# Performance work log

Measured on AMD Instinct MI355X. Metric: run time of the kernel, lower is better.

The kernel has to match this reference:

```python
import jax, jax.numpy as jnp
import numpy as np


def setup_inputs() -> dict:
    key = jax.random.key(0)
    ks = jax.random.split(key, 6)
    B, F, C = 2048, 512, 64
    t_feat = jax.random.normal(ks[0], (B, F), dtype=jnp.float32)
    f_feat = jax.random.normal(ks[1], (B, F), dtype=jnp.float32)
    # proj Linear(F*F -> C); scale like torch default init (~1/sqrt(fan_in))
    W_proj = jax.random.normal(ks[2], (C, F * F), dtype=jnp.float32) / np.sqrt(F * F)
    b_proj = jnp.zeros((C,), dtype=jnp.float32)
    W1 = jax.random.normal(ks[3], (32, C), dtype=jnp.float32) / np.sqrt(C)
    b1 = jnp.zeros((32,), dtype=jnp.float32)
    W2 = jax.random.normal(ks[4], (1, 32), dtype=jnp.float32) / np.sqrt(32)
    b2 = jnp.zeros((1,), dtype=jnp.float32)
    return {"t_feat": t_feat, "f_feat": f_feat, "W_proj": W_proj, "b_proj": b_proj,
            "W1": W1, "b1": b1, "W2": W2, "b2": b2}


def reference(t_feat, f_feat, W_proj, b_proj, W1, b1, W2, b2):
    B, F = t_feat.shape
    C = W_proj.shape[0]
    # corr[b,i,j] = t[b,i] * f[b,j]; proj = corr_flat @ W_proj.T + b_proj.
    # Equivalent bilinear form computed WITHOUT materializing the (B,F,F) outer product:
    Wr = W_proj.reshape(C, F, F)            # W_proj[c, i*F + j] -> Wr[c,i,j]
    tmp = jnp.einsum('bi,cij->bcj', t_feat, Wr)   # (B, C, F)
    proj = jnp.einsum('bcj,bj->bc', tmp, f_feat) + b_proj  # (B, C)
    h = jax.nn.relu(proj)
    # GRL is identity in forward
    h2 = jax.nn.relu(h @ W1.T + b1)          # (B, 32)
    logit = h2 @ W2.T + b2                   # (B, 1)
    return logit
```

## Files before the change

### kernel.cpp

```cpp
#include <hip/hip_runtime.h>
#include <hip/hip_bf16.h>
#include <stdint.h>

#define BATCH 2048
#define FDIM 512
#define CDIM 64

typedef unsigned short ushort_t;
typedef __attribute__((ext_vector_type(8))) short short8;
typedef __attribute__((ext_vector_type(4))) float f32x4;

__device__ __forceinline__ ushort_t f2bf(float x) {
    union { float f; uint32_t u; } v; v.f = x;
    uint32_t u = v.u;
    uint32_t r = u + 0x7FFFu + ((u >> 16) & 1u);
    return (ushort_t)(r >> 16);
}
__device__ __forceinline__ float bf2f(ushort_t u) {
    union { float f; uint32_t v; } x; x.v = ((uint32_t)u) << 16; return x.f;
}

__global__ void convert_kernel(const float* __restrict__ src, ushort_t* __restrict__ dst) {
    int idx = blockIdx.x * 256 + threadIdx.x;
    float4 v0 = ((const float4*)src)[idx * 2];
    float4 v1 = ((const float4*)src)[idx * 2 + 1];
    ushort_t p[8] = { f2bf(v0.x), f2bf(v0.y), f2bf(v0.z), f2bf(v0.w),
                      f2bf(v1.x), f2bf(v1.y), f2bf(v1.z), f2bf(v1.w) };
    *(uint4*)&dst[idx * 8] = *(uint4*)p;
}

__global__ void convert_ft_kernel(const float* __restrict__ f, ushort_t* __restrict__ f16,
                                  const float* __restrict__ t, ushort_t* __restrict__ t16) {
    int blk = blockIdx.x;
    const float* src = (blk < 512) ? f : t;
    ushort_t* dst    = (blk < 512) ? f16 : t16;
    int idx = (blk & 511) * 256 + threadIdx.x;
    float4 v0 = ((const float4*)src)[idx * 2];
    float4 v1 = ((const float4*)src)[idx * 2 + 1];
    ushort_t p[8] = { f2bf(v0.x), f2bf(v0.y), f2bf(v0.z), f2bf(v0.w),
                      f2bf(v1.x), f2bf(v1.y), f2bf(v1.z), f2bf(v1.w) };
    *(uint4*)&dst[idx * 8] = *(uint4*)p;
}

#define AS3(p) ((__attribute__((address_space(3))) void*)(p))
#define AS1(p) ((const __attribute__((address_space(1))) void*)(p))

__launch_bounds__(256, 2)
__global__ void gemm_fused_kernel(const ushort_t* __restrict__ f16,
                                  const ushort_t* __restrict__ Wb,
                                  const ushort_t* __restrict__ t16,
                                  float* __restrict__ part) {
    __shared__ ushort_t As[128 * 32];
    __shared__ ushort_t Bs[128 * 32];
    __shared__ float scratch[256];

    const int tid  = threadIdx.x;
    const int wave = tid >> 6;
    const int lane = tid & 63;
    const int l15  = lane & 15;
    const int lg   = lane >> 4;

    const int b0 = blockIdx.x * 128;
    const int n0 = blockIdx.y * 128;

    const int m_base = (wave >> 1) * 64;
    const int nh     = wave & 1;
    const int n_base = nh * 64;

    f32x4 acc[4][4];
    #pragma unroll
    for (int mi = 0; mi < 4; mi++)
        #pragma unroll
        for (int ni = 0; ni < 4; ni++)
            acc[mi][ni] = (f32x4){0.f, 0.f, 0.f, 0.f};

    const int p    = tid >> 2;
    const int cph  = tid & 3;
    const int cg   = cph ^ ((p >> 1) & 3);
    const int nrot = ((p & 15) << 2) | (p >> 4);

    const ushort_t* gA0 = f16 + (size_t)(b0 + p) * FDIM + cg * 8;
    const ushort_t* gA1 = f16 + (size_t)(b0 + 64 + p) * FDIM + cg * 8;
    const ushort_t* gB0 = Wb + (size_t)(n0 + nrot) * FDIM + cg * 8;
    const ushort_t* gB1 = Wb + (size_t)(n0 + 64 + nrot) * FDIM + cg * 8;

    for (int k0 = 0; k0 < FDIM; k0 += 32) {
        __builtin_amdgcn_global_load_lds(AS1(gA0 + k0), AS3(&As[0 * 2048 + wave * 512]), 16, 0, 0);
        __builtin_amdgcn_global_load_lds(AS1(gA1 + k0), AS3(&As[1 * 2048 + wave * 512]), 16, 0, 0);
        __builtin_amdgcn_global_load_lds(AS1(gB0 + k0), AS3(&Bs[0 * 2048 + wave * 512]), 16, 0, 0);
        __builtin_amdgcn_global_load_lds(AS1(gB1 + k0), AS3(&Bs[1 * 2048 + wave * 512]), 16, 0, 0);
        __syncthreads();

        short8 a[4], b[4];
        #pragma unroll
        for (int mi = 0; mi < 4; mi++) {
            int r = m_base + mi * 16 + l15;
            a[mi] = *(const short8*)&As[r * 32 + (lg ^ ((r >> 1) & 3)) * 8];
        }
        #pragma unroll
        for (int ni = 0; ni < 4; ni++) {
            int q = n_base + ni * 16 + l15;
            b[ni] = *(const short8*)&Bs[q * 32 + (lg ^ ((q >> 1) & 3)) * 8];
        }

        #pragma unroll
        for (int mi = 0; mi < 4; mi++)
            #pragma unroll
            for (int ni = 0; ni < 4; ni++)
                acc[mi][ni] = __builtin_amdgcn_mfma_f32_16x16x32_bf16(a[mi], b[ni], acc[mi][ni], 0, 0, 0);

        __syncthreads();
    }

    const int c  = n0 >> 9;
    const int iq = (n0 >> 7) & 3;
    const int i_base = (n0 & 511) + n_base + l15 * 4;

    #pragma unroll
    for (int mi = 0; mi < 4; mi++) {
        #pragma unroll
        for (int r = 0; r < 4; r++) {
            int b_idx = b0 + m_base + mi * 16 + lg * 4 + r;
            ushort4 tv = *(const ushort4*)&t16[(size_t)b_idx * FDIM + i_base];
            float sv = acc[mi][0][r] * bf2f(tv.x) + acc[mi][1][r] * bf2f(tv.y)
                     + acc[mi][2][r] * bf2f(tv.z) + acc[mi][3][r] * bf2f(tv.w);
            sv += __shfl_xor(sv, 1, 64);
            sv += __shfl_xor(sv, 2, 64);
            sv += __shfl_xor(sv, 4, 64);
            sv += __shfl_xor(sv, 8, 64);
            if (l15 == 0)
                scratch[(m_base + mi * 16 + lg * 4 + r) * 2 + nh] = sv;
        }
    }
    __syncthreads();
    if (tid < 128) {
        float v = scratch[tid * 2] + scratch[tid * 2 + 1];
        part[(((size_t)(b0 + tid)) * 64 + c) * 4 + iq] = v;
    }
}

__global__ void mlp_kernel(const float* __restrict__ part,
                           const float* __restrict__ b_proj,
                           const float* __restrict__ W1, const float* __restrict__ b1,
                           const float* __restrict__ W2, const float* __restrict__ b2,
                           float* __restrict__ out) {
    __shared__ float h[8][64];
    const int tid = threadIdx.x;
    const int bl  = tid >> 5;
    const int o   = tid & 31;
    const int b   = blockIdx.x * 8 + bl;

    #pragma unroll
    for (int c = o; c < 64; c += 32) {
        float4 v = *(const float4*)&part[(((size_t)b * 64 + c)) * 4];
        float sv = v.x + v.y + v.z + v.w + b_proj[c];
        h[bl][c] = sv > 0.f ? sv : 0.f;
    }
    __syncthreads();

    float sv = b1[o];
    #pragma unroll
    for (int c = 0; c < 64; c++) sv += h[bl][c] * W1[o * 64 + c];
    float v = (sv > 0.f ? sv : 0.f) * W2[o];
    v += __shfl_xor(v, 1, 32);
    v += __shfl_xor(v, 2, 32);
    v += __shfl_xor(v, 4, 32);
    v += __shfl_xor(v, 8, 32);
    v += __shfl_xor(v, 16, 32);
    if (o == 0) out[b] = v + b2[0];
}

extern "C" void kernel_launch(void* const* d_in, const int* in_sizes, int n_in,
                              void* d_out, int out_size, void* d_ws, size_t ws_size,
                              hipStream_t stream) {
    const float* t_feat = (const float*)d_in[0];
    const float* f_feat = (const float*)d_in[1];
    const float* W_proj = (const float*)d_in[2];
    const float* b_proj = (const float*)d_in[3];
    const float* W1     = (const float*)d_in[4];
    const float* b1     = (const float*)d_in[5];
    const float* W2     = (const float*)d_in[6];
    const float* b2     = (const float*)d_in[7];
    float* out = (float*)d_out;

    uint8_t* ws = (uint8_t*)d_ws;
    ushort_t* Wb   = (ushort_t*)(ws);
    ushort_t* f16  = (ushort_t*)(ws + 33554432);
    ushort_t* t16  = (ushort_t*)(ws + 33554432 + 2097152);
    float*    part = (float*)(ws + 33554432 + 2 * 2097152);

    convert_kernel<<<dim3((CDIM * FDIM * FDIM) / 2048), dim3(256), 0, stream>>>(W_proj, Wb);
    convert_ft_kernel<<<dim3(1024), dim3(256), 0, stream>>>(f_feat, f16, t_feat, t16);

    gemm_fused_kernel<<<dim3(BATCH / 128, (CDIM * FDIM) / 128), dim3(256), 0, stream>>>(
        f16, Wb, t16, part);

    mlp_kernel<<<dim3(BATCH / 8), dim3(256), 0, stream>>>(part, b_proj, W1, b1, W2, b2, out);
}
```

Baseline: 211.1 us.

## Double-buffer 256x256 GEMM tiles with phased prefetch and merge conversion kernels

The GEMM moves from 128x128 tiles with a single LDS buffer to 256x256 tiles run by 8 waves. It double-buffers BK=64 k-tiles and issues the global-to-LDS prefetch of the next tile inside phases interleaved with the MFMA work, using explicit barriers, waitcnt and setprio. A block-index swizzle improves L2 reuse, the three conversion kernels are merged into one launch, and the partial-sum layout shrinks from four to two slices per channel. The aim is to hide load latency behind compute and raise arithmetic intensity, at the cost of more registers and LDS (64KB+) and fragile hand scheduling.

```diff
diff --git a/kernel.cpp b/kernel.cpp
--- a/kernel.cpp
+++ b/kernel.cpp
@@ -5,6 +5,8 @@
 #define BATCH 2048
 #define FDIM 512
 #define CDIM 64
+#define BK 64
+#define NKT (FDIM / BK)
 
 typedef unsigned short ushort_t;
 typedef __attribute__((ext_vector_type(8))) short short8;
@@ -20,8 +22,14 @@
     union { float f; uint32_t v; } x; x.v = ((uint32_t)u) << 16; return x.f;
 }
 
-__global__ void convert_kernel(const float* __restrict__ src, ushort_t* __restrict__ dst) {
-    int idx = blockIdx.x * 256 + threadIdx.x;
+__global__ void convert_all_kernel(const float* __restrict__ W, ushort_t* __restrict__ Wb,
+                                   const float* __restrict__ f, ushort_t* __restrict__ f16,
+                                   const float* __restrict__ t, ushort_t* __restrict__ t16) {
+    int blk = blockIdx.x;
+    const float* src; ushort_t* dst; int idx;
+    if (blk < 8192)      { src = W; dst = Wb;  idx = blk * 256 + threadIdx.x; }
+    else if (blk < 8704) { src = f; dst = f16; idx = (blk - 8192) * 256 + threadIdx.x; }
+    else                 { src = t; dst = t16; idx = (blk - 8704) * 256 + threadIdx.x; }
     float4 v0 = ((const float4*)src)[idx * 2];
     float4 v1 = ((const float4*)src)[idx * 2 + 1];
     ushort_t p[8] = { f2bf(v0.x), f2bf(v0.y), f2bf(v0.z), f2bf(v0.w),
@@ -29,113 +37,149 @@
     *(uint4*)&dst[idx * 8] = *(uint4*)p;
 }
 
-__global__ void convert_ft_kernel(const float* __restrict__ f, ushort_t* __restrict__ f16,
-                                  const float* __restrict__ t, ushort_t* __restrict__ t16) {
-    int blk = blockIdx.x;
-    const float* src = (blk < 512) ? f : t;
-    ushort_t* dst    = (blk < 512) ? f16 : t16;
-    int idx = (blk & 511) * 256 + threadIdx.x;
-    float4 v0 = ((const float4*)src)[idx * 2];
-    float4 v1 = ((const float4*)src)[idx * 2 + 1];
-    ushort_t p[8] = { f2bf(v0.x), f2bf(v0.y), f2bf(v0.z), f2bf(v0.w),
-                      f2bf(v1.x), f2bf(v1.y), f2bf(v1.z), f2bf(v1.w) };
-    *(uint4*)&dst[idx * 8] = *(uint4*)p;
-}
-
 #define AS3(p) ((__attribute__((address_space(3))) void*)(p))
 #define AS1(p) ((const __attribute__((address_space(1))) void*)(p))
 
-__launch_bounds__(256, 2)
+
+#define STAGE_A(buf, ksub, kelem)                                                   \
+    { _Pragma("unroll")                                                             \
+      for (int l = 0; l < 2; l++)                                                   \
+        __builtin_amdgcn_global_load_lds(AS1(gA[l] + (kelem) + (ksub) * 32),        \
+            AS3(&AsB[buf][ksub][l * 4096 + wave * 512]), 16, 0, 0); }
+
+#define STAGE_B(buf, ksub, kelem)                                                   \
+    { _Pragma("unroll")                                                             \
+      for (int l = 0; l < 2; l++)                                                   \
+        __builtin_amdgcn_global_load_lds(AS1(gB[l] + (kelem) + (ksub) * 32),        \
+            AS3(&BsB[buf][ksub][l * 4096 + wave * 512]), 16, 0, 0); }
+
+#define LOADB4(buf, ksub)                                                           \
+    { _Pragma("unroll")                                                             \
+      for (int ni = 0; ni < 4; ni++)                                                \
+        bv[ni] = *(const short8*)&BsB[buf][ksub][b_off[ni]]; }
+
+#define VMW4 asm volatile("s_waitcnt vmcnt(4)" ::: "memory");
+
+#define PHASE(buf, ksub, mibase, EXTRA, STG, VMW)                                   \
+    { _Pragma("unroll")                                                             \
+      for (int mi = 0; mi < 4; mi++)                                                \
+        av[mi] = *(const short8*)&AsB[buf][ksub][a_off[(mibase) + mi]];             \
+      EXTRA                                                                         \
+      STG                                                                           \
+      __builtin_amdgcn_s_barrier();                                                 \
+      asm volatile("s_waitcnt lgkmcnt(0)" ::: "memory");                            \
+      __builtin_amdgcn_sched_barrier(0);                                            \
+      __builtin_amdgcn_s_setprio(1);                                                \
+      _Pragma("unroll")                                                             \
+      for (int mi = 0; mi < 4; mi++) {                                              \
+        _Pragma("unroll")                                                           \
+        for (int ni = 0; ni < 4; ni++)                                              \
+          acc[(mibase) + mi][ni] = __builtin_amdgcn_mfma_f32_16x16x32_bf16(         \
+              av[mi], bv[ni], acc[(mibase) + mi][ni], 0, 0, 0);                     \
+      }                                                                             \
+      __builtin_amdgcn_s_setprio(0);                                                \
+      VMW                                                                           \
+      __builtin_amdgcn_s_barrier();                                                 \
+      asm volatile("" ::: "memory"); }
+
+#define DO_KTILE(buf, nk)                                                           \
+    PHASE(buf, 0, 0, LOADB4(buf, 0), STAGE_A((buf) ^ 1, 0, nk), )                   \
+    PHASE(buf, 0, 4, , STAGE_B((buf) ^ 1, 0, nk), VMW4)                             \
+    PHASE(buf, 1, 0, LOADB4(buf, 1), STAGE_A((buf) ^ 1, 1, nk), )                   \
+    PHASE(buf, 1, 4, , STAGE_B((buf) ^ 1, 1, nk), VMW4)
+
+__launch_bounds__(512, 2)
 __global__ void gemm_fused_kernel(const ushort_t* __restrict__ f16,
                                   const ushort_t* __restrict__ Wb,
                                   const ushort_t* __restrict__ t16,
                                   float* __restrict__ part) {
-    __shared__ ushort_t As[128 * 32];
-    __shared__ ushort_t Bs[128 * 32];
-    __shared__ float scratch[256];
+    __shared__ ushort_t AsB[2][2][256 * 32];
+    __shared__ ushort_t BsB[2][2][256 * 32];
+    __shared__ float scratch[256 * 4];
 
     const int tid  = threadIdx.x;
     const int wave = tid >> 6;
     const int lane = tid & 63;
     const int l15  = lane & 15;
     const int lg   = lane >> 4;
-
-    const int b0 = blockIdx.x * 128;
-    const int n0 = blockIdx.y * 128;
-
-    const int m_base = (wave >> 1) * 64;
-    const int nh     = wave & 1;
-    const int n_base = nh * 64;
-
-    f32x4 acc[4][4];
-    #pragma unroll
-    for (int mi = 0; mi < 4; mi++)
+    const int wm   = wave >> 2;
+    const int wn   = wave & 3;
+
+    const int swz = (blockIdx.x & 7) * 128 + (blockIdx.x >> 3);
+    const int by  = swz >> 3;
+    const int bx  = swz & 7;
+    const int b0  = bx * 256;
+    const int n0  = by * 256;
+
+    const ushort_t* gA[2];
+    const ushort_t* gB[2];
+    #pragma unroll
+    for (int l = 0; l < 2; l++) {
+        int s   = l * 512 + tid;
+        int row = s >> 2;
+        int cg  = (s & 3) ^ ((row >> 1) & 3);
+        gA[l] = f16 + (size_t)(b0 + row) * FDIM + cg * 8;
+        int bq = (row & ~63) | ((row & 15) << 2) | ((row >> 4) & 3);
+        gB[l] = Wb + (size_t)(n0 + bq) * FDIM + cg * 8;
+    }
+
+    int a_off[8], b_off[4];
+    const int cx = (lg ^ ((l15 >> 1) & 3)) * 8;
+    #pragma unroll
+    for (int mi = 0; mi < 8; mi++) {
+        int r = wm * 128 + mi * 16 + l15;
+        a_off[mi] = r * 32 + cx;
+    }
+    #pragma unroll
+    for (int ni = 0; ni < 4; ni++) {
+        int q = wn * 64 + ni * 16 + l15;
+        b_off[ni] = q * 32 + cx;
+    }
+
+    f32x4 acc[8][4];
+    #pragma unroll
+    for (int mi = 0; mi < 8; mi++)
         #pragma unroll
         for (int ni = 0; ni < 4; ni++)
             acc[mi][ni] = (f32x4){0.f, 0.f, 0.f, 0.f};
 
-    const int p    = tid >> 2;
-    const int cph  = tid & 3;
-    const int cg   = cph ^ ((p >> 1) & 3);
-    const int nrot = ((p & 15) << 2) | (p >> 4);
-
-    const ushort_t* gA0 = f16 + (size_t)(b0 + p) * FDIM + cg * 8;
-    const ushort_t* gA1 = f16 + (size_t)(b0 + 64 + p) * FDIM + cg * 8;
-    const ushort_t* gB0 = Wb + (size_t)(n0 + nrot) * FDIM + cg * 8;
-    const ushort_t* gB1 = Wb + (size_t)(n0 + 64 + nrot) * FDIM + cg * 8;
-
-    for (int k0 = 0; k0 < FDIM; k0 += 32) {
-        __builtin_amdgcn_global_load_lds(AS1(gA0 + k0), AS3(&As[0 * 2048 + wave * 512]), 16, 0, 0);
-        __builtin_amdgcn_global_load_lds(AS1(gA1 + k0), AS3(&As[1 * 2048 + wave * 512]), 16, 0, 0);
-        __builtin_amdgcn_global_load_lds(AS1(gB0 + k0), AS3(&Bs[0 * 2048 + wave * 512]), 16, 0, 0);
-        __builtin_amdgcn_global_load_lds(AS1(gB1 + k0), AS3(&Bs[1 * 2048 + wave * 512]), 16, 0, 0);
-        __syncthreads();
-
-        short8 a[4], b[4];
-        #pragma unroll
-        for (int mi = 0; mi < 4; mi++) {
-            int r = m_base + mi * 16 + l15;
-            a[mi] = *(const short8*)&As[r * 32 + (lg ^ ((r >> 1) & 3)) * 8];
-        }
-        #pragma unroll
-        for (int ni = 0; ni < 4; ni++) {
-            int q = n_base + ni * 16 + l15;
-            b[ni] = *(const short8*)&Bs[q * 32 + (lg ^ ((q >> 1) & 3)) * 8];
-        }
-
-        #pragma unroll
-        for (int mi = 0; mi < 4; mi++)
-            #pragma unroll
-            for (int ni = 0; ni < 4; ni++)
-                acc[mi][ni] = __builtin_amdgcn_mfma_f32_16x16x32_bf16(a[mi], b[ni], acc[mi][ni], 0, 0, 0);
-
-        __syncthreads();
-    }
-
-    const int c  = n0 >> 9;
-    const int iq = (n0 >> 7) & 3;
-    const int i_base = (n0 & 511) + n_base + l15 * 4;
-
-    #pragma unroll
-    for (int mi = 0; mi < 4; mi++) {
+    short8 av[4], bv[4];
+
+    STAGE_A(0, 0, 0)
+    STAGE_B(0, 0, 0)
+    STAGE_A(0, 1, 0)
+    STAGE_B(0, 1, 0)
+    __syncthreads();
+
+    for (int kt2 = 0; kt2 < 4; kt2++) {
+        const int nk1 = (kt2 * 2 + 1) * BK;
+        const int nk2 = (kt2 < 3) ? (kt2 * 2 + 2) * BK : 0;
+        DO_KTILE(0, nk1)
+        DO_KTILE(1, nk2)
+    }
+
+    const int c     = n0 >> 9;
+    const int half  = (n0 >> 8) & 1;
+    const int ibase = (n0 & 511) + wn * 64 + l15 * 4;
+    #pragma unroll
+    for (int mi = 0; mi < 8; mi++) {
+        const int row_blk = wm * 128 + mi * 16 + lg * 4;
         #pragma unroll
         for (int r = 0; r < 4; r++) {
-            int b_idx = b0 + m_base + mi * 16 + lg * 4 + r;
-            ushort4 tv = *(const ushort4*)&t16[(size_t)b_idx * FDIM + i_base];
+            ushort4 tv = *(const ushort4*)&t16[(size_t)(b0 + row_blk + r) * FDIM + ibase];
             float sv = acc[mi][0][r] * bf2f(tv.x) + acc[mi][1][r] * bf2f(tv.y)
                      + acc[mi][2][r] * bf2f(tv.z) + acc[mi][3][r] * bf2f(tv.w);
             sv += __shfl_xor(sv, 1, 64);
             sv += __shfl_xor(sv, 2, 64);
             sv += __shfl_xor(sv, 4, 64);
             sv += __shfl_xor(sv, 8, 64);
-            if (l15 == 0)
-                scratch[(m_base + mi * 16 + lg * 4 + r) * 2 + nh] = sv;
+            if (l15 == 0) scratch[(row_blk + r) * 4 + wn] = sv;
         }
     }
     __syncthreads();
-    if (tid < 128) {
-        float v = scratch[tid * 2] + scratch[tid * 2 + 1];
-        part[(((size_t)(b0 + tid)) * 64 + c) * 4 + iq] = v;
+    if (tid < 256) {
+        float4 s4 = *(const float4*)&scratch[tid * 4];
+        part[((size_t)(b0 + tid) * CDIM + c) * 2 + half] = s4.x + s4.y + s4.z + s4.w;
     }
 }
 
@@ -152,8 +196,8 @@
 
     #pragma unroll
     for (int c = o; c < 64; c += 32) {
-        float4 v = *(const float4*)&part[(((size_t)b * 64 + c)) * 4];
-        float sv = v.x + v.y + v.z + v.w + b_proj[c];
+        float2 v = *(const float2*)&part[((size_t)b * 64 + c) * 2];
+        float sv = v.x + v.y + b_proj[c];
         h[bl][c] = sv > 0.f ? sv : 0.f;
     }
     __syncthreads();
@@ -189,11 +233,9 @@
     ushort_t* t16  = (ushort_t*)(ws + 33554432 + 2097152);
     float*    part = (float*)(ws + 33554432 + 2 * 2097152);
 
-    convert_kernel<<<dim3((CDIM * FDIM * FDIM) / 2048), dim3(256), 0, stream>>>(W_proj, Wb);
-    convert_ft_kernel<<<dim3(1024), dim3(256), 0, stream>>>(f_feat, f16, t_feat, t16);
-
-    gemm_fused_kernel<<<dim3(BATCH / 128, (CDIM * FDIM) / 128), dim3(256), 0, stream>>>(
-        f16, Wb, t16, part);
+    convert_all_kernel<<<dim3(9216), dim3(256), 0, stream>>>(W_proj, Wb, f_feat, f16, t_feat, t16);
+
+    gemm_fused_kernel<<<dim3(1024), dim3(512), 0, stream>>>(f16, Wb, t16, part);
 
     mlp_kernel<<<dim3(BATCH / 8), dim3(256), 0, stream>>>(part, b_proj, W1, b1, W2, b2, out);
 }
```

After: 237.3 us. 1.12x slower.

## Load GEMM operands straight to registers with double buffering, XCD-aware block mapping, merged conversions

Applied to the files above, without the earlier changes.

Drops the LDS staging in the bilinear GEMM. Each wave now loads its A and B fragments directly from global memory into registers, double-buffered across K steps, with no barriers inside the K loop. Blocks are remapped onto a 1D grid so that each XCD takes a contiguous range of W column tiles for L2 reuse, and occupancy is raised to 3 blocks per CU. The two fp32-to-bf16 conversion kernels are merged into one launch. In exchange, the per-wave global loads are redundant and less coalesced (the 16-byte B row loads are strided), and register pressure rises.

```diff
diff --git a/kernel.cpp b/kernel.cpp
--- a/kernel.cpp
+++ b/kernel.cpp
@@ -20,8 +20,14 @@
     union { float f; uint32_t v; } x; x.v = ((uint32_t)u) << 16; return x.f;
 }
 
-__global__ void convert_kernel(const float* __restrict__ src, ushort_t* __restrict__ dst) {
-    int idx = blockIdx.x * 256 + threadIdx.x;
+__global__ void convert_all_kernel(const float* __restrict__ W, ushort_t* __restrict__ Wb,
+                                   const float* __restrict__ f, ushort_t* __restrict__ f16,
+                                   const float* __restrict__ t, ushort_t* __restrict__ t16) {
+    int blk = blockIdx.x;
+    const float* src; ushort_t* dst; int idx;
+    if (blk < 8192)      { src = W; dst = Wb;  idx = blk * 256 + threadIdx.x; }
+    else if (blk < 8704) { src = f; dst = f16; idx = (blk - 8192) * 256 + threadIdx.x; }
+    else                 { src = t; dst = t16; idx = (blk - 8704) * 256 + threadIdx.x; }
     float4 v0 = ((const float4*)src)[idx * 2];
     float4 v1 = ((const float4*)src)[idx * 2 + 1];
     ushort_t p[8] = { f2bf(v0.x), f2bf(v0.y), f2bf(v0.z), f2bf(v0.w),
@@ -29,43 +35,52 @@
     *(uint4*)&dst[idx * 8] = *(uint4*)p;
 }
 
-__global__ void convert_ft_kernel(const float* __restrict__ f, ushort_t* __restrict__ f16,
-                                  const float* __restrict__ t, ushort_t* __restrict__ t16) {
-    int blk = blockIdx.x;
-    const float* src = (blk < 512) ? f : t;
-    ushort_t* dst    = (blk < 512) ? f16 : t16;
-    int idx = (blk & 511) * 256 + threadIdx.x;
-    float4 v0 = ((const float4*)src)[idx * 2];
-    float4 v1 = ((const float4*)src)[idx * 2 + 1];
-    ushort_t p[8] = { f2bf(v0.x), f2bf(v0.y), f2bf(v0.z), f2bf(v0.w),
-                      f2bf(v1.x), f2bf(v1.y), f2bf(v1.z), f2bf(v1.w) };
-    *(uint4*)&dst[idx * 8] = *(uint4*)p;
-}
 
-#define AS3(p) ((__attribute__((address_space(3))) void*)(p))
-#define AS1(p) ((const __attribute__((address_space(1))) void*)(p))
+#define LOADK(Ad, Bd, koff)                                                         \
+    { _Pragma("unroll")                                                             \
+      for (int mi = 0; mi < 4; mi++) Ad[mi] = *(const short8*)(pA[mi] + (koff));    \
+      _Pragma("unroll")                                                             \
+      for (int ni = 0; ni < 4; ni++) Bd[ni] = *(const short8*)(pB[ni] + (koff)); }
 
-__launch_bounds__(256, 2)
+#define MFMAK(Av, Bv)                                                               \
+    { _Pragma("unroll")                                                             \
+      for (int mi = 0; mi < 4; mi++) {                                              \
+        _Pragma("unroll")                                                           \
+        for (int ni = 0; ni < 4; ni++)                                              \
+          acc[mi][ni] = __builtin_amdgcn_mfma_f32_16x16x32_bf16(                    \
+              Av[mi], Bv[ni], acc[mi][ni], 0, 0, 0);                                \
+      } }
+
+__launch_bounds__(256, 3)
 __global__ void gemm_fused_kernel(const ushort_t* __restrict__ f16,
                                   const ushort_t* __restrict__ Wb,
                                   const ushort_t* __restrict__ t16,
                                   float* __restrict__ part) {
-    __shared__ ushort_t As[128 * 32];
-    __shared__ ushort_t Bs[128 * 32];
-    __shared__ float scratch[256];
+    __shared__ float scratch[128 * 2];
 
     const int tid  = threadIdx.x;
     const int wave = tid >> 6;
     const int lane = tid & 63;
     const int l15  = lane & 15;
     const int lg   = lane >> 4;
+    const int wm   = wave >> 1;
+    const int wn   = wave & 1;
 
-    const int b0 = blockIdx.x * 128;
-    const int n0 = blockIdx.y * 128;
+    const int xcd = blockIdx.x & 7;
+    const int idx = blockIdx.x >> 3;
+    const int bx  = idx & 15;
+    const int by  = xcd * 32 + (idx >> 4);
+    const int b0  = bx * 128;
+    const int n0  = by * 128;
 
-    const int m_base = (wave >> 1) * 64;
-    const int nh     = wave & 1;
-    const int n_base = nh * 64;
+    const ushort_t* pA[4];
+    const ushort_t* pB[4];
+    #pragma unroll
+    for (int mi = 0; mi < 4; mi++)
+        pA[mi] = f16 + (size_t)(b0 + wm * 64 + mi * 16 + l15) * FDIM + lg * 8;
+    #pragma unroll
+    for (int ni = 0; ni < 4; ni++)
+        pB[ni] = Wb + (size_t)(n0 + wn * 64 + l15 * 4 + ni) * FDIM + lg * 8;
 
     f32x4 acc[4][4];
     #pragma unroll
@@ -74,68 +89,39 @@
         for (int ni = 0; ni < 4; ni++)
             acc[mi][ni] = (f32x4){0.f, 0.f, 0.f, 0.f};
 
-    const int p    = tid >> 2;
-    const int cph  = tid & 3;
-    const int cg   = cph ^ ((p >> 1) & 3);
-    const int nrot = ((p & 15) << 2) | (p >> 4);
+    short8 A0[4], B0[4], A1[4], B1[4];
 
-    const ushort_t* gA0 = f16 + (size_t)(b0 + p) * FDIM + cg * 8;
-    const ushort_t* gA1 = f16 + (size_t)(b0 + 64 + p) * FDIM + cg * 8;
-    const ushort_t* gB0 = Wb + (size_t)(n0 + nrot) * FDIM + cg * 8;
-    const ushort_t* gB1 = Wb + (size_t)(n0 + 64 + nrot) * FDIM + cg * 8;
-
-    for (int k0 = 0; k0 < FDIM; k0 += 32) {
-        __builtin_amdgcn_global_load_lds(AS1(gA0 + k0), AS3(&As[0 * 2048 + wave * 512]), 16, 0, 0);
-        __builtin_amdgcn_global_load_lds(AS1(gA1 + k0), AS3(&As[1 * 2048 + wave * 512]), 16, 0, 0);
-        __builtin_amdgcn_global_load_lds(AS1(gB0 + k0), AS3(&Bs[0 * 2048 + wave * 512]), 16, 0, 0);
-        __builtin_amdgcn_global_load_lds(AS1(gB1 + k0), AS3(&Bs[1 * 2048 + wave * 512]), 16, 0, 0);
-        __syncthreads();
-
-        short8 a[4], b[4];
-        #pragma unroll
-        for (int mi = 0; mi < 4; mi++) {
-            int r = m_base + mi * 16 + l15;
-            a[mi] = *(const short8*)&As[r * 32 + (lg ^ ((r >> 1) & 3)) * 8];
-        }
-        #pragma unroll
-        for (int ni = 0; ni < 4; ni++) {
-            int q = n_base + ni * 16 + l15;
-            b[ni] = *(const short8*)&Bs[q * 32 + (lg ^ ((q >> 1) & 3)) * 8];
-        }
-
-        #pragma unroll
-        for (int mi = 0; mi < 4; mi++)
-            #pragma unroll
-            for (int ni = 0; ni < 4; ni++)
-                acc[mi][ni] = __builtin_amdgcn_mfma_f32_16x16x32_bf16(a[mi], b[ni], acc[mi][ni], 0, 0, 0);
-
-        __syncthreads();
+    LOADK(A0, B0, 0)
+    #pragma unroll 1
+    for (int k = 0; k < FDIM; k += 64) {
+        LOADK(A1, B1, k + 32)
+        MFMAK(A0, B0)
+        LOADK(A0, B0, (k + 64) & 511)
+        MFMAK(A1, B1)
     }
 
-    const int c  = n0 >> 9;
-    const int iq = (n0 >> 7) & 3;
-    const int i_base = (n0 & 511) + n_base + l15 * 4;
-
+    const int c      = n0 >> 9;
+    const int iq     = (n0 >> 7) & 3;
+    const int i_base = (n0 & 511) + wn * 64 + l15 * 4;
     #pragma unroll
     for (int mi = 0; mi < 4; mi++) {
+        const int row_blk = wm * 64 + mi * 16 + lg * 4;
         #pragma unroll
         for (int r = 0; r < 4; r++) {
-            int b_idx = b0 + m_base + mi * 16 + lg * 4 + r;
-            ushort4 tv = *(const ushort4*)&t16[(size_t)b_idx * FDIM + i_base];
+            ushort4 tv = *(const ushort4*)&t16[(size_t)(b0 + row_blk + r) * FDIM + i_base];
             float sv = acc[mi][0][r] * bf2f(tv.x) + acc[mi][1][r] * bf2f(tv.y)
                      + acc[mi][2][r] * bf2f(tv.z) + acc[mi][3][r] * bf2f(tv.w);
             sv += __shfl_xor(sv, 1, 64);
             sv += __shfl_xor(sv, 2, 64);
             sv += __shfl_xor(sv, 4, 64);
             sv += __shfl_xor(sv, 8, 64);
-            if (l15 == 0)
-                scratch[(m_base + mi * 16 + lg * 4 + r) * 2 + nh] = sv;
+            if (l15 == 0) scratch[(row_blk + r) * 2 + wn] = sv;
         }
     }
     __syncthreads();
     if (tid < 128) {
-        float v = scratch[tid * 2] + scratch[tid * 2 + 1];
-        part[(((size_t)(b0 + tid)) * 64 + c) * 4 + iq] = v;
+        float2 s2 = *(const float2*)&scratch[tid * 2];
+        part[(((size_t)(b0 + tid)) * CDIM + c) * 4 + iq] = s2.x + s2.y;
     }
 }
 
@@ -189,10 +175,9 @@
     ushort_t* t16  = (ushort_t*)(ws + 33554432 + 2097152);
     float*    part = (float*)(ws + 33554432 + 2 * 2097152);
 
-    convert_kernel<<<dim3((CDIM * FDIM * FDIM) / 2048), dim3(256), 0, stream>>>(W_proj, Wb);
-    convert_ft_kernel<<<dim3(1024), dim3(256), 0, stream>>>(f_feat, f16, t_feat, t16);
+    convert_all_kernel<<<dim3(9216), dim3(256), 0, stream>>>(W_proj, Wb, f_feat, f16, t_feat, t16);
 
-    gemm_fused_kernel<<<dim3(BATCH / 128, (CDIM * FDIM) / 128), dim3(256), 0, stream>>>(
+    gemm_fused_kernel<<<dim3((BATCH / 128) * ((CDIM * FDIM) / 128)), dim3(256), 0, stream>>>(
         f16, Wb, t16, part);
 
     mlp_kernel<<<dim3(BATCH / 8), dim3(256), 0, stream>>>(part, b_proj, W1, b1, W2, b2, out);
```

New measurement: 355.9 us. 1.69x slower.

## Double-buffer GEMM LDS tiles, remap blocks per XCD, merge convert kernels

Applied to the files above, without the earlier changes.

The GEMM main loop now uses two LDS buffers, so the global-to-LDS loads for the next K tile are issued before the MFMAs on the current tile, and each step needs one barrier instead of two. The grid is flattened to 1D and remapped so each XCD gets a contiguous range of W_proj column tiles, which should improve L2 reuse of the weight tiles. Launch bounds rise to 4 blocks per CU, which limits register use. The three fp32-to-bf16 conversion launches are merged into one kernel to save launch overhead. The extra LDS and the tighter register budget could lower occupancy or cause spills.

```diff
diff --git a/kernel.cpp b/kernel.cpp
--- a/kernel.cpp
+++ b/kernel.cpp
@@ -20,8 +20,14 @@
     union { float f; uint32_t v; } x; x.v = ((uint32_t)u) << 16; return x.f;
 }
 
-__global__ void convert_kernel(const float* __restrict__ src, ushort_t* __restrict__ dst) {
-    int idx = blockIdx.x * 256 + threadIdx.x;
+__global__ void convert_all_kernel(const float* __restrict__ W, ushort_t* __restrict__ Wb,
+                                   const float* __restrict__ f, ushort_t* __restrict__ f16,
+                                   const float* __restrict__ t, ushort_t* __restrict__ t16) {
+    int blk = blockIdx.x;
+    const float* src; ushort_t* dst; int idx;
+    if (blk < 8192)      { src = W; dst = Wb;  idx = blk * 256 + threadIdx.x; }
+    else if (blk < 8704) { src = f; dst = f16; idx = (blk - 8192) * 256 + threadIdx.x; }
+    else                 { src = t; dst = t16; idx = (blk - 8704) * 256 + threadIdx.x; }
     float4 v0 = ((const float4*)src)[idx * 2];
     float4 v1 = ((const float4*)src)[idx * 2 + 1];
     ushort_t p[8] = { f2bf(v0.x), f2bf(v0.y), f2bf(v0.z), f2bf(v0.w),
@@ -29,29 +35,37 @@
     *(uint4*)&dst[idx * 8] = *(uint4*)p;
 }
 
-__global__ void convert_ft_kernel(const float* __restrict__ f, ushort_t* __restrict__ f16,
-                                  const float* __restrict__ t, ushort_t* __restrict__ t16) {
-    int blk = blockIdx.x;
-    const float* src = (blk < 512) ? f : t;
-    ushort_t* dst    = (blk < 512) ? f16 : t16;
-    int idx = (blk & 511) * 256 + threadIdx.x;
-    float4 v0 = ((const float4*)src)[idx * 2];
-    float4 v1 = ((const float4*)src)[idx * 2 + 1];
-    ushort_t p[8] = { f2bf(v0.x), f2bf(v0.y), f2bf(v0.z), f2bf(v0.w),
-                      f2bf(v1.x), f2bf(v1.y), f2bf(v1.z), f2bf(v1.w) };
-    *(uint4*)&dst[idx * 8] = *(uint4*)p;
-}
-
 #define AS3(p) ((__attribute__((address_space(3))) void*)(p))
 #define AS1(p) ((const __attribute__((address_space(1))) void*)(p))
 
-__launch_bounds__(256, 2)
+
+#define STAGE(bi, kt)                                                               \
+    __builtin_amdgcn_global_load_lds(AS1(gA0 + (kt) * 32), AS3(&As[bi][0 * 2048 + wave * 512]), 16, 0, 0); \
+    __builtin_amdgcn_global_load_lds(AS1(gA1 + (kt) * 32), AS3(&As[bi][1 * 2048 + wave * 512]), 16, 0, 0); \
+    __builtin_amdgcn_global_load_lds(AS1(gB0 + (kt) * 32), AS3(&Bs[bi][0 * 2048 + wave * 512]), 16, 0, 0); \
+    __builtin_amdgcn_global_load_lds(AS1(gB1 + (kt) * 32), AS3(&Bs[bi][1 * 2048 + wave * 512]), 16, 0, 0);
+
+#define COMPUTE(bi)                                                                 \
+    { short8 a[4], b[4];                                                            \
+      _Pragma("unroll")                                                             \
+      for (int mi = 0; mi < 4; mi++) a[mi] = *(const short8*)&As[bi][a_off[mi]];    \
+      _Pragma("unroll")                                                             \
+      for (int ni = 0; ni < 4; ni++) b[ni] = *(const short8*)&Bs[bi][b_off[ni]];    \
+      _Pragma("unroll")                                                             \
+      for (int mi = 0; mi < 4; mi++) {                                              \
+        _Pragma("unroll")                                                           \
+        for (int ni = 0; ni < 4; ni++)                                              \
+          acc[mi][ni] = __builtin_amdgcn_mfma_f32_16x16x32_bf16(                    \
+              a[mi], b[ni], acc[mi][ni], 0, 0, 0);                                  \
+      } }
+
+__launch_bounds__(256, 4)
 __global__ void gemm_fused_kernel(const ushort_t* __restrict__ f16,
                                   const ushort_t* __restrict__ Wb,
                                   const ushort_t* __restrict__ t16,
                                   float* __restrict__ part) {
-    __shared__ ushort_t As[128 * 32];
-    __shared__ ushort_t Bs[128 * 32];
+    __shared__ ushort_t As[2][128 * 32];
+    __shared__ ushort_t Bs[2][128 * 32];
     __shared__ float scratch[256];
 
     const int tid  = threadIdx.x;
@@ -60,12 +74,38 @@
     const int l15  = lane & 15;
     const int lg   = lane >> 4;
 
-    const int b0 = blockIdx.x * 128;
-    const int n0 = blockIdx.y * 128;
-
     const int m_base = (wave >> 1) * 64;
     const int nh     = wave & 1;
     const int n_base = nh * 64;
+
+    const int xcd = blockIdx.x & 7;
+    const int idx = blockIdx.x >> 3;
+    const int bx  = idx & 15;
+    const int by  = xcd * 32 + (idx >> 4);
+    const int b0  = bx * 128;
+    const int n0  = by * 128;
+
+    const int p    = tid >> 2;
+    const int cph  = tid & 3;
+    const int cg   = cph ^ ((p >> 1) & 3);
+    const int nrot = ((p & 15) << 2) | (p >> 4);
+
+    const ushort_t* gA0 = f16 + (size_t)(b0 + p) * FDIM + cg * 8;
+    const ushort_t* gA1 = f16 + (size_t)(b0 + 64 + p) * FDIM + cg * 8;
+    const ushort_t* gB0 = Wb + (size_t)(n0 + nrot) * FDIM + cg * 8;
+    const ushort_t* gB1 = Wb + (size_t)(n0 + 64 + nrot) * FDIM + cg * 8;
+
+    int a_off[4], b_off[4];
+    #pragma unroll
+    for (int mi = 0; mi < 4; mi++) {
+        int r = m_base + mi * 16 + l15;
+        a_off[mi] = r * 32 + (lg ^ ((r >> 1) & 3)) * 8;
+    }
+    #pragma unroll
+    for (int ni = 0; ni < 4; ni++) {
+        int q = n_base + ni * 16 + l15;
+        b_off[ni] = q * 32 + (lg ^ ((q >> 1) & 3)) * 8;
+    }
 
     f32x4 acc[4][4];
     #pragma unroll
@@ -74,43 +114,16 @@
         for (int ni = 0; ni < 4; ni++)
             acc[mi][ni] = (f32x4){0.f, 0.f, 0.f, 0.f};
 
-    const int p    = tid >> 2;
-    const int cph  = tid & 3;
-    const int cg   = cph ^ ((p >> 1) & 3);
-    const int nrot = ((p & 15) << 2) | (p >> 4);
-
-    const ushort_t* gA0 = f16 + (size_t)(b0 + p) * FDIM + cg * 8;
-    const ushort_t* gA1 = f16 + (size_t)(b0 + 64 + p) * FDIM + cg * 8;
-    const ushort_t* gB0 = Wb + (size_t)(n0 + nrot) * FDIM + cg * 8;
-    const ushort_t* gB1 = Wb + (size_t)(n0 + 64 + nrot) * FDIM + cg * 8;
-
-    for (int k0 = 0; k0 < FDIM; k0 += 32) {
-        __builtin_amdgcn_global_load_lds(AS1(gA0 + k0), AS3(&As[0 * 2048 + wave * 512]), 16, 0, 0);
-        __builtin_amdgcn_global_load_lds(AS1(gA1 + k0), AS3(&As[1 * 2048 + wave * 512]), 16, 0, 0);
-        __builtin_amdgcn_global_load_lds(AS1(gB0 + k0), AS3(&Bs[0 * 2048 + wave * 512]), 16, 0, 0);
-        __builtin_amdgcn_global_load_lds(AS1(gB1 + k0), AS3(&Bs[1 * 2048 + wave * 512]), 16, 0, 0);
-        __syncthreads();
-
-        short8 a[4], b[4];
-        #pragma unroll
-        for (int mi = 0; mi < 4; mi++) {
-            int r = m_base + mi * 16 + l15;
-            a[mi] = *(const short8*)&As[r * 32 + (lg ^ ((r >> 1) & 3)) * 8];
-        }
-        #pragma unroll
-        for (int ni = 0; ni < 4; ni++) {
-            int q = n_base + ni * 16 + l15;
-            b[ni] = *(const short8*)&Bs[q * 32 + (lg ^ ((q >> 1) & 3)) * 8];
-        }
-
-        #pragma unroll
-        for (int mi = 0; mi < 4; mi++)
-            #pragma unroll
-            for (int ni = 0; ni < 4; ni++)
-                acc[mi][ni] = __builtin_amdgcn_mfma_f32_16x16x32_bf16(a[mi], b[ni], acc[mi][ni], 0, 0, 0);
-
-        __syncthreads();
-    }
+    STAGE(0, 0)
+    __syncthreads();
+    #pragma unroll 1
+    for (int t2 = 0; t2 < 7; t2++) {
+        const int kt = t2 * 2;
+        STAGE(1, kt + 1) COMPUTE(0) __syncthreads();
+        STAGE(0, kt + 2) COMPUTE(1) __syncthreads();
+    }
+    STAGE(1, 15) COMPUTE(0) __syncthreads();
+    COMPUTE(1)
 
     const int c  = n0 >> 9;
     const int iq = (n0 >> 7) & 3;
@@ -189,10 +202,9 @@
     ushort_t* t16  = (ushort_t*)(ws + 33554432 + 2097152);
     float*    part = (float*)(ws + 33554432 + 2 * 2097152);
 
-    convert_kernel<<<dim3((CDIM * FDIM * FDIM) / 2048), dim3(256), 0, stream>>>(W_proj, Wb);
-    convert_ft_kernel<<<dim3(1024), dim3(256), 0, stream>>>(f_feat, f16, t_feat, t16);
-
-    gemm_fused_kernel<<<dim3(BATCH / 128, (CDIM * FDIM) / 128), dim3(256), 0, stream>>>(
+    convert_all_kernel<<<dim3(9216), dim3(256), 0, stream>>>(W_proj, Wb, f_feat, f16, t_feat, t16);
+
+    gemm_fused_kernel<<<dim3((BATCH / 128) * ((CDIM * FDIM) / 128)), dim3(256), 0, stream>>>(
         f16, Wb, t16, part);
 
     mlp_kernel<<<dim3(BATCH / 8), dim3(256), 0, stream>>>(part, b_proj, W1, b1, W2, b2, out);
```

Result: no change. 209.6 us (-0.7%).
